# Kernel tuning notes

Measured on AMD Instinct MI355X. Metric: run time of the kernel, lower is better.

## Reference

```python
import jax, jax.numpy as jnp
import numpy as np
from functools import partial

FS = 30.0
CUTOFF = 3.3
ORDER = 5
PADLEN = 18  # scipy filtfilt default: 3 * max(len(a), len(b)) = 3 * 6


def butter_lowpass_np(order, Wn):
    """Digital Butterworth lowpass (b, a), matching scipy.signal.butter."""
    # analog prototype poles (buttap)
    m = np.arange(-order + 1, order, 2)
    p = -np.exp(1j * np.pi * m / (2 * order))
    k = 1.0
    # pre-warp frequency (scipy uses internal fs = 2.0)
    fs = 2.0
    warped = 2 * fs * np.tan(np.pi * Wn / fs)
    p = warped * p
    k = k * warped ** order
    # bilinear transform
    fs2 = 2 * fs
    p_z = (fs2 + p) / (fs2 - p)
    z_z = -np.ones(order)
    k_z = k * np.real(1.0 / np.prod(fs2 - p))
    b = k_z * np.real(np.poly(z_z))
    a = np.real(np.poly(p_z))
    return b.astype(np.float64), a.astype(np.float64)


def lfilter_zi_np(b, a):
    """Steady-state initial conditions, matching scipy.signal.lfilter_zi."""
    n = len(a)
    comp = np.zeros((n - 1, n - 1))
    comp[0, :] = -a[1:] / a[0]
    if n > 2:
        comp[1:, :-1] = np.eye(n - 2)
    B = b[1:] - a[1:] * b[0]
    return np.linalg.solve(np.eye(n - 1) - comp.T, B)


def lfilter(b, a, x, zi):
    """Direct-form II transposed IIR filter along a 1-D signal via lax.scan."""
    def step(z, xt):
        y = b[0] * xt + z[0]
        z_shift = jnp.concatenate([z[1:], jnp.zeros(1, z.dtype)])
        z_new = b[1:] * xt + z_shift - a[1:] * y
        return z_new, y
    _, y = jax.lax.scan(step, zi, x)
    return y


def filtfilt_1d(b, a, zi, x):
    """Zero-phase filtering with odd-extension padding (scipy filtfilt defaults)."""
    left = 2 * x[0] - x[PADLEN:0:-1]
    right = 2 * x[-1] - x[-2:-(PADLEN + 2):-1]
    ext = jnp.concatenate([left, x, right])
    y = lfilter(b, a, ext, zi * ext[0])
    y = lfilter(b, a, y[::-1], zi * y[-1])[::-1]
    return y[PADLEN:-PADLEN]


def setup_inputs() -> dict:
    key = jax.random.key(0)
    x = jax.random.normal(key, (4096, 8192), dtype=jnp.float32)
    Wn = CUTOFF / (FS / 2.0)
    b_np, a_np = butter_lowpass_np(ORDER, Wn)
    zi_np = lfilter_zi_np(b_np, a_np)
    return {
        "x": x,
        "b": jnp.asarray(b_np, dtype=jnp.float32),
        "a": jnp.asarray(a_np, dtype=jnp.float32),
        "zi": jnp.asarray(zi_np, dtype=jnp.float32),
    }


def reference(x, b, a, zi):
    # batched zero-phase Butterworth lowpass, [batch, length] -> [batch, length]
    return jax.vmap(partial(filtfilt_1d, b, a, zi))(x)
```

## Files before the change

### kernel.cpp

```cpp
#include <hip/hip_runtime.h>


#define NN   8192
#define PADL 18
#define LC   32
#define TPB  256

__device__ __forceinline__ int xw(int c, int i) {
    return (i << 8) + (c ^ (((i >> 2) & 7) << 2));
}

#define STEP(xv) do {                               \
    float y_ = fmaf(b0, (xv), z0);                  \
    z0 = fmaf(na1, y_, fmaf(b1, (xv), z1));         \
    z1 = fmaf(na2, y_, fmaf(b2, (xv), z2));         \
    z2 = fmaf(na3, y_, fmaf(b3, (xv), z3));         \
    z3 = fmaf(na4, y_, fmaf(b4, (xv), z4));         \
    z4 = fmaf(na5, y_, b5 * (xv));                  \
    yv = y_;                                        \
} while (0)

__global__ __launch_bounds__(TPB, 4) void GREEN_62869731278967_filtfilt(
    const float* __restrict__ x,
    const float* __restrict__ bc,
    const float* __restrict__ ac,
    const float* __restrict__ zc,
    float* __restrict__ out)
{
    __shared__ float lds[NN];
    const int row = blockIdx.x;
    const int tid = threadIdx.x;
    const float* xr   = x   + (size_t)row * NN;
    float*       outr = out + (size_t)row * NN;

    const float b0 = bc[0], b1 = bc[1], b2 = bc[2], b3 = bc[3], b4 = bc[4], b5 = bc[5];
    const float na1 = -ac[1], na2 = -ac[2], na3 = -ac[3], na4 = -ac[4], na5 = -ac[5];
    const float zi0 = zc[0], zi1 = zc[1], zi2 = zc[2], zi3 = zc[3], zi4 = zc[4];

    {
        const int Abase = ((tid & 7) << 10) + ((tid >> 3) ^ ((tid & 7) << 2));
#pragma unroll
        for (int q = 0; q < 8; ++q) {
            float4 v = *reinterpret_cast<const float4*>(xr + (q << 10) + (tid << 2));
            lds[Abase + (q << 5) + 0]   = v.x;
            lds[Abase + (q << 5) + 256] = v.y;
            lds[Abase + (q << 5) + 512] = v.z;
            lds[Abase + (q << 5) + 768] = v.w;
        }
    }
    __syncthreads();

    float yreg[LC];
    float ynx[LC];
    float z0, z1, z2, z3, z4, yv;

    if (tid == 0) {
        const float x0 = lds[xw(0, 0)];
        float v0 = 2.f * x0 - lds[xw(0, PADL)];
        z0 = zi0 * v0; z1 = zi1 * v0; z2 = zi2 * v0; z3 = zi3 * v0; z4 = zi4 * v0;
#pragma unroll
        for (int t = 0; t < PADL; ++t) {
            float v = 2.f * x0 - lds[xw(0, PADL - t)];
            STEP(v);
        }
    } else {
        float v0 = lds[xw(tid - 1, 0)];
        z0 = zi0 * v0; z1 = zi1 * v0; z2 = zi2 * v0; z3 = zi3 * v0; z4 = zi4 * v0;
#pragma unroll
        for (int i = 0; i < LC; ++i) STEP(lds[xw(tid - 1, i)]);
    }
#pragma unroll
    for (int i = 0; i < LC; ++i) { STEP(lds[xw(tid, i)]); yreg[i] = yv; }
    if (tid < TPB - 1) {
#pragma unroll
        for (int i = 0; i < LC; ++i) { STEP(lds[xw(tid + 1, i)]); ynx[i] = yv; }
    } else {
        const float xN = lds[xw(TPB - 1, 31)];
#pragma unroll
        for (int i = 0; i < PADL; ++i) {
            float v = 2.f * xN - lds[xw(TPB - 1, 30 - i)];
            STEP(v);
            ynx[i] = yv;
        }
    }

    if (tid == TPB - 1) {
        float u0 = ynx[PADL - 1];
        z0 = zi0 * u0; z1 = zi1 * u0; z2 = zi2 * u0; z3 = zi3 * u0; z4 = zi4 * u0;
#pragma unroll
        for (int s = 0; s < PADL; ++s) STEP(ynx[PADL - 1 - s]);
    } else {
        float u0 = ynx[LC - 1];
        z0 = zi0 * u0; z1 = zi1 * u0; z2 = zi2 * u0; z3 = zi3 * u0; z4 = zi4 * u0;
#pragma unroll
        for (int i = 0; i < LC; ++i) STEP(ynx[LC - 1 - i]);
    }
#pragma unroll
    for (int i = 0; i < LC; ++i) { STEP(yreg[LC - 1 - i]); yreg[LC - 1 - i] = yv; }

#pragma unroll
    for (int q = 0; q < LC / 4; ++q) {
        float4 v;
        v.x = yreg[4 * q + 0];
        v.y = yreg[4 * q + 1];
        v.z = yreg[4 * q + 2];
        v.w = yreg[4 * q + 3];
        *reinterpret_cast<float4*>(outr + tid * LC + 4 * q) = v;
    }
}

extern "C" void kernel_launch(void* const* d_in, const int* in_sizes, int n_in,
                              void* d_out, int out_size, void* d_ws, size_t ws_size,
                              hipStream_t stream) {
    const float* x  = (const float*)d_in[0];
    const float* b  = (const float*)d_in[1];
    const float* a  = (const float*)d_in[2];
    const float* zi = (const float*)d_in[3];
    float* out = (float*)d_out;
    const int rows = in_sizes[0] / NN;
    GREEN_62869731278967_filtfilt<<<rows, TPB, 0, stream>>>(x, b, a, zi, out);
}
```

Measured before the change: 65.63 us.

## Process four rows per block with register prefetch and LDS-shared forward results

Each block now handles four rows, prefetching the next row's input into registers while filtering the current one. Instead of every thread recomputing its right neighbour's forward pass, forward outputs are written to LDS and the backward warmup reads them from there. This halves that redundant forward work and hides global load latency, at the cost of extra barriers, more registers for the prefetch buffer, and a quarter as many blocks, which reduces parallelism across the GPU.

```diff
diff --git a/kernel.cpp b/kernel.cpp
--- a/kernel.cpp
+++ b/kernel.cpp
@@ -5,6 +5,7 @@
 #define PADL 18
 #define LC   32
 #define TPB  256
+#define ROWS 4
 
 __device__ __forceinline__ int xw(int c, int i) {
     return (i << 8) + (c ^ (((i >> 2) & 7) << 2));
@@ -28,84 +29,102 @@
     float* __restrict__ out)
 {
     __shared__ float lds[NN];
-    const int row = blockIdx.x;
     const int tid = threadIdx.x;
-    const float* xr   = x   + (size_t)row * NN;
-    float*       outr = out + (size_t)row * NN;
+    const int row0 = blockIdx.x * ROWS;
 
     const float b0 = bc[0], b1 = bc[1], b2 = bc[2], b3 = bc[3], b4 = bc[4], b5 = bc[5];
     const float na1 = -ac[1], na2 = -ac[2], na3 = -ac[3], na4 = -ac[4], na5 = -ac[5];
     const float zi0 = zc[0], zi1 = zc[1], zi2 = zc[2], zi3 = zc[3], zi4 = zc[4];
 
+    const int Abase = ((tid & 7) << 10) + ((tid >> 3) ^ ((tid & 7) << 2));
+
+    float4 xnx[8];
     {
-        const int Abase = ((tid & 7) << 10) + ((tid >> 3) ^ ((tid & 7) << 2));
+        const float* xr = x + (size_t)row0 * NN;
+#pragma unroll
+        for (int q = 0; q < 8; ++q)
+            xnx[q] = *reinterpret_cast<const float4*>(xr + (q << 10) + (tid << 2));
+    }
+
+#pragma unroll 1
+    for (int r = 0; r < ROWS; ++r) {
+        float*       outr = out + (size_t)(row0 + r) * NN;
+
+        __syncthreads();
 #pragma unroll
         for (int q = 0; q < 8; ++q) {
-            float4 v = *reinterpret_cast<const float4*>(xr + (q << 10) + (tid << 2));
-            lds[Abase + (q << 5) + 0]   = v.x;
-            lds[Abase + (q << 5) + 256] = v.y;
-            lds[Abase + (q << 5) + 512] = v.z;
-            lds[Abase + (q << 5) + 768] = v.w;
+            lds[Abase + (q << 5) + 0]   = xnx[q].x;
+            lds[Abase + (q << 5) + 256] = xnx[q].y;
+            lds[Abase + (q << 5) + 512] = xnx[q].z;
+            lds[Abase + (q << 5) + 768] = xnx[q].w;
         }
-    }
-    __syncthreads();
+        __syncthreads();
 
-    float yreg[LC];
-    float ynx[LC];
-    float z0, z1, z2, z3, z4, yv;
+        if (r + 1 < ROWS) {
+            const float* xr = x + (size_t)(row0 + r + 1) * NN;
+#pragma unroll
+            for (int q = 0; q < 8; ++q)
+                xnx[q] = *reinterpret_cast<const float4*>(xr + (q << 10) + (tid << 2));
+        }
 
-    if (tid == 0) {
-        const float x0 = lds[xw(0, 0)];
-        float v0 = 2.f * x0 - lds[xw(0, PADL)];
-        z0 = zi0 * v0; z1 = zi1 * v0; z2 = zi2 * v0; z3 = zi3 * v0; z4 = zi4 * v0;
+        float yreg[LC];
+        float ytail[PADL];
+        float z0, z1, z2, z3, z4, yv;
+        if (tid == 0) {
+            const float x0 = lds[xw(0, 0)];
+            float v0 = 2.f * x0 - lds[xw(0, PADL)];
+            z0 = zi0 * v0; z1 = zi1 * v0; z2 = zi2 * v0; z3 = zi3 * v0; z4 = zi4 * v0;
 #pragma unroll
-        for (int t = 0; t < PADL; ++t) {
-            float v = 2.f * x0 - lds[xw(0, PADL - t)];
-            STEP(v);
+            for (int t = 0; t < PADL; ++t) {
+                float v = 2.f * x0 - lds[xw(0, PADL - t)];
+                STEP(v);
+            }
+        } else {
+            float v0 = lds[xw(tid - 1, 0)];
+            z0 = zi0 * v0; z1 = zi1 * v0; z2 = zi2 * v0; z3 = zi3 * v0; z4 = zi4 * v0;
+#pragma unroll
+            for (int i = 0; i < LC; ++i) STEP(lds[xw(tid - 1, i)]);
         }
-    } else {
-        float v0 = lds[xw(tid - 1, 0)];
-        z0 = zi0 * v0; z1 = zi1 * v0; z2 = zi2 * v0; z3 = zi3 * v0; z4 = zi4 * v0;
 #pragma unroll
-        for (int i = 0; i < LC; ++i) STEP(lds[xw(tid - 1, i)]);
-    }
+        for (int i = 0; i < LC; ++i) { STEP(lds[xw(tid, i)]); yreg[i] = yv; }
+        if (tid == TPB - 1) {
+            const float xN = lds[xw(TPB - 1, 31)];
 #pragma unroll
-    for (int i = 0; i < LC; ++i) { STEP(lds[xw(tid, i)]); yreg[i] = yv; }
-    if (tid < TPB - 1) {
-#pragma unroll
-        for (int i = 0; i < LC; ++i) { STEP(lds[xw(tid + 1, i)]); ynx[i] = yv; }
-    } else {
-        const float xN = lds[xw(TPB - 1, 31)];
-#pragma unroll
-        for (int i = 0; i < PADL; ++i) {
-            float v = 2.f * xN - lds[xw(TPB - 1, 30 - i)];
-            STEP(v);
-            ynx[i] = yv;
+            for (int i = 0; i < PADL; ++i) {
+                float v = 2.f * xN - lds[xw(TPB - 1, 30 - i)];
+                STEP(v);
+                ytail[i] = yv;
+            }
         }
-    }
-
-    if (tid == TPB - 1) {
-        float u0 = ynx[PADL - 1];
-        z0 = zi0 * u0; z1 = zi1 * u0; z2 = zi2 * u0; z3 = zi3 * u0; z4 = zi4 * u0;
-#pragma unroll
-        for (int s = 0; s < PADL; ++s) STEP(ynx[PADL - 1 - s]);
-    } else {
-        float u0 = ynx[LC - 1];
-        z0 = zi0 * u0; z1 = zi1 * u0; z2 = zi2 * u0; z3 = zi3 * u0; z4 = zi4 * u0;
-#pragma unroll
-        for (int i = 0; i < LC; ++i) STEP(ynx[LC - 1 - i]);
-    }
-#pragma unroll
-    for (int i = 0; i < LC; ++i) { STEP(yreg[LC - 1 - i]); yreg[LC - 1 - i] = yv; }
+        __syncthreads();
 
 #pragma unroll
-    for (int q = 0; q < LC / 4; ++q) {
-        float4 v;
-        v.x = yreg[4 * q + 0];
-        v.y = yreg[4 * q + 1];
-        v.z = yreg[4 * q + 2];
-        v.w = yreg[4 * q + 3];
-        *reinterpret_cast<float4*>(outr + tid * LC + 4 * q) = v;
+        for (int i = 0; i < LC; ++i) lds[xw(tid, i)] = yreg[i];
+        __syncthreads();
+
+        if (tid == TPB - 1) {
+            float u0 = ytail[PADL - 1];
+            z0 = zi0 * u0; z1 = zi1 * u0; z2 = zi2 * u0; z3 = zi3 * u0; z4 = zi4 * u0;
+#pragma unroll
+            for (int s = 0; s < PADL; ++s) STEP(ytail[PADL - 1 - s]);
+        } else {
+            float u0 = lds[xw(tid + 1, LC - 1)];
+            z0 = zi0 * u0; z1 = zi1 * u0; z2 = zi2 * u0; z3 = zi3 * u0; z4 = zi4 * u0;
+#pragma unroll
+            for (int i = 0; i < LC; ++i) STEP(lds[xw(tid + 1, LC - 1 - i)]);
+        }
+#pragma unroll
+        for (int i = 0; i < LC; ++i) { STEP(yreg[LC - 1 - i]); yreg[LC - 1 - i] = yv; }
+
+#pragma unroll
+        for (int q = 0; q < LC / 4; ++q) {
+            float4 v;
+            v.x = yreg[4 * q + 0];
+            v.y = yreg[4 * q + 1];
+            v.z = yreg[4 * q + 2];
+            v.w = yreg[4 * q + 3];
+            *reinterpret_cast<float4*>(outr + tid * LC + 4 * q) = v;
+        }
     }
 }
 
@@ -118,5 +137,6 @@
     const float* zi = (const float*)d_in[3];
     float* out = (float*)d_out;
     const int rows = in_sizes[0] / NN;
-    GREEN_62869731278967_filtfilt<<<rows, TPB, 0, stream>>>(x, b, a, zi, out);
+    const int blocks = rows / ROWS;
+    GREEN_62869731278967_filtfilt<<<blocks, TPB, 0, stream>>>(x, b, a, zi, out);
 }
```

New measurement: 70.62 us. 7.6% more time.

## Share forward-pass outputs via LDS and load input with global_load_lds

Applied to the files above, without the earlier changes.

The input row now goes straight into LDS through the async global_load_lds builtin, using an XOR-swizzled chunk-major layout that allows float4 LDS reads. The forward pass no longer recomputes the next thread's chunk to get backward warm-up values. Each thread writes its forward outputs to LDS after a barrier, and the neighbour reads them back for the backward warm-up. This removes about a third of the serial IIR steps per thread, in exchange for extra barriers, LDS writes, and a dependency on the builtin's lane-to-address mapping being correct.

```diff
diff --git a/kernel.cpp b/kernel.cpp
--- a/kernel.cpp
+++ b/kernel.cpp
@@ -1,4 +1,5 @@
 #include <hip/hip_runtime.h>
+#include <stdint.h>
 
 
 #define NN   8192
@@ -6,8 +7,22 @@
 #define LC   32
 #define TPB  256
 
-__device__ __forceinline__ int xw(int c, int i) {
-    return (i << 8) + (c ^ (((i >> 2) & 7) << 2));
+typedef uint32_t u32;
+
+__device__ __forceinline__ void gload16(const float* g, float* l) {
+    __builtin_amdgcn_global_load_lds(
+        (const __attribute__((address_space(1))) u32*)g,
+        (__attribute__((address_space(3))) u32*)l, 16, 0, 0);
+}
+
+__device__ __forceinline__ float SC(const float* lds, int c, int e) {
+    return lds[(c << 5) + (((e >> 2) ^ (c & 7)) << 2) + (e & 3)];
+}
+__device__ __forceinline__ float4 LDQ(const float* lds, int c, int j) {
+    return *reinterpret_cast<const float4*>(lds + (c << 5) + ((j ^ (c & 7)) << 2));
+}
+__device__ __forceinline__ void STQ(float* lds, int c, int j, float4 v) {
+    *reinterpret_cast<float4*>(lds + (c << 5) + ((j ^ (c & 7)) << 2)) = v;
 }
 
 #define STEP(xv) do {                               \
@@ -38,62 +53,76 @@
     const float zi0 = zc[0], zi1 = zc[1], zi2 = zc[2], zi3 = zc[3], zi4 = zc[4];
 
     {
-        const int Abase = ((tid & 7) << 10) + ((tid >> 3) ^ ((tid & 7) << 2));
+        const int wv = tid >> 6, L = tid & 63;
+        const float* srow = xr + ((wv << 11) + ((L >> 3) << 5) + (((L & 7) ^ (L >> 3)) << 2));
+        float* lbase = lds + (wv << 11);
 #pragma unroll
-        for (int q = 0; q < 8; ++q) {
-            float4 v = *reinterpret_cast<const float4*>(xr + (q << 10) + (tid << 2));
-            lds[Abase + (q << 5) + 0]   = v.x;
-            lds[Abase + (q << 5) + 256] = v.y;
-            lds[Abase + (q << 5) + 512] = v.z;
-            lds[Abase + (q << 5) + 768] = v.w;
+        for (int k = 0; k < 8; ++k)
+            gload16(srow + (k << 8), lbase + (k << 8));
+    }
+    asm volatile("s_waitcnt vmcnt(0)" ::: "memory");
+    __syncthreads();
+
+    float yreg[LC];
+    float ytail[PADL];
+    float z0, z1, z2, z3, z4, yv;
+
+    if (tid == 0) {
+        const float x0 = lds[0];
+        float v0 = 2.f * x0 - lds[PADL];
+        z0 = zi0 * v0; z1 = zi1 * v0; z2 = zi2 * v0; z3 = zi3 * v0; z4 = zi4 * v0;
+#pragma unroll
+        for (int t = 0; t < PADL; ++t) {
+            float v = 2.f * x0 - lds[PADL - t];
+            STEP(v);
+        }
+    } else {
+        float v0 = SC(lds, tid - 1, 0);
+        z0 = zi0 * v0; z1 = zi1 * v0; z2 = zi2 * v0; z3 = zi3 * v0; z4 = zi4 * v0;
+#pragma unroll
+        for (int j = 0; j < 8; ++j) {
+            float4 q = LDQ(lds, tid - 1, j);
+            STEP(q.x); STEP(q.y); STEP(q.z); STEP(q.w);
+        }
+    }
+#pragma unroll
+    for (int j = 0; j < 8; ++j) {
+        float4 q = LDQ(lds, tid, j);
+        STEP(q.x); yreg[4 * j + 0] = yv;
+        STEP(q.y); yreg[4 * j + 1] = yv;
+        STEP(q.z); yreg[4 * j + 2] = yv;
+        STEP(q.w); yreg[4 * j + 3] = yv;
+    }
+    if (tid == TPB - 1) {
+        const float xN = SC(lds, TPB - 1, 31);
+#pragma unroll
+        for (int i = 0; i < PADL; ++i) {
+            float v = 2.f * xN - SC(lds, TPB - 1, 30 - i);
+            STEP(v);
+            ytail[i] = yv;
         }
     }
     __syncthreads();
 
-    float yreg[LC];
-    float ynx[LC];
-    float z0, z1, z2, z3, z4, yv;
-
-    if (tid == 0) {
-        const float x0 = lds[xw(0, 0)];
-        float v0 = 2.f * x0 - lds[xw(0, PADL)];
-        z0 = zi0 * v0; z1 = zi1 * v0; z2 = zi2 * v0; z3 = zi3 * v0; z4 = zi4 * v0;
 #pragma unroll
-        for (int t = 0; t < PADL; ++t) {
-            float v = 2.f * x0 - lds[xw(0, PADL - t)];
-            STEP(v);
-        }
-    } else {
-        float v0 = lds[xw(tid - 1, 0)];
-        z0 = zi0 * v0; z1 = zi1 * v0; z2 = zi2 * v0; z3 = zi3 * v0; z4 = zi4 * v0;
-#pragma unroll
-        for (int i = 0; i < LC; ++i) STEP(lds[xw(tid - 1, i)]);
-    }
-#pragma unroll
-    for (int i = 0; i < LC; ++i) { STEP(lds[xw(tid, i)]); yreg[i] = yv; }
-    if (tid < TPB - 1) {
-#pragma unroll
-        for (int i = 0; i < LC; ++i) { STEP(lds[xw(tid + 1, i)]); ynx[i] = yv; }
-    } else {
-        const float xN = lds[xw(TPB - 1, 31)];
-#pragma unroll
-        for (int i = 0; i < PADL; ++i) {
-            float v = 2.f * xN - lds[xw(TPB - 1, 30 - i)];
-            STEP(v);
-            ynx[i] = yv;
-        }
-    }
+    for (int j = 0; j < 8; ++j)
+        STQ(lds, tid, j, make_float4(yreg[4 * j], yreg[4 * j + 1],
+                                     yreg[4 * j + 2], yreg[4 * j + 3]));
+    __syncthreads();
 
     if (tid == TPB - 1) {
-        float u0 = ynx[PADL - 1];
+        float u0 = ytail[PADL - 1];
         z0 = zi0 * u0; z1 = zi1 * u0; z2 = zi2 * u0; z3 = zi3 * u0; z4 = zi4 * u0;
 #pragma unroll
-        for (int s = 0; s < PADL; ++s) STEP(ynx[PADL - 1 - s]);
+        for (int s = 0; s < PADL; ++s) STEP(ytail[PADL - 1 - s]);
     } else {
-        float u0 = ynx[LC - 1];
+        float u0 = SC(lds, tid + 1, LC - 1);
         z0 = zi0 * u0; z1 = zi1 * u0; z2 = zi2 * u0; z3 = zi3 * u0; z4 = zi4 * u0;
 #pragma unroll
-        for (int i = 0; i < LC; ++i) STEP(ynx[LC - 1 - i]);
+        for (int j = 7; j >= 0; --j) {
+            float4 q = LDQ(lds, tid + 1, j);
+            STEP(q.w); STEP(q.z); STEP(q.y); STEP(q.x);
+        }
     }
 #pragma unroll
     for (int i = 0; i < LC; ++i) { STEP(yreg[LC - 1 - i]); yreg[LC - 1 - i] = yv; }
```

After: 65.24 us. No clear change (-0.6%).
